# Optimization experiments

Measured on AMD Instinct MI355X. Metric: run time of the kernel, lower is better.

The kernel has to match this reference:

```python
import jax, jax.numpy as jnp
import numpy as np

B, L, E, H, D = 4, 2048, 2048, 16, 128
HALF = D // 2
EPS = 1e-6


def setup_inputs() -> dict:
    key = jax.random.key(0)
    ks = jax.random.split(key, 8)
    s = 1.0 / np.sqrt(E)
    x = jax.random.normal(ks[0], (B, L, E), dtype=jnp.float32)
    # causal boolean mask, True = attend
    attention_mask = jnp.tril(jnp.ones((L, L), dtype=bool))[None, None, :, :]
    attention_mask = jnp.broadcast_to(attention_mask, (B, 1, L, L))
    pos = jnp.arange(L, dtype=jnp.float32)[:, None]
    inv_freq = 1.0 / (10000.0 ** (jnp.arange(HALF, dtype=jnp.float32) / HALF))
    ang = pos * inv_freq[None, :]  # [L, HALF]
    cos = jnp.broadcast_to(jnp.cos(ang)[None], (B, L, HALF)).astype(jnp.float32)
    sin = jnp.broadcast_to(jnp.sin(ang)[None], (B, L, HALF)).astype(jnp.float32)
    Wq = jax.random.normal(ks[1], (H * D, E), dtype=jnp.float32) * s
    Wk = jax.random.normal(ks[2], (H * D, E), dtype=jnp.float32) * s
    Wv = jax.random.normal(ks[3], (H * D, E), dtype=jnp.float32) * s
    Wo = jax.random.normal(ks[4], (E, H * D), dtype=jnp.float32) * s
    q_norm_w = jnp.ones((D,), dtype=jnp.float32)
    k_norm_w = jnp.ones((D,), dtype=jnp.float32)
    return {"x": x, "attention_mask": attention_mask, "cos": cos, "sin": sin,
            "Wq": Wq, "Wk": Wk, "Wv": Wv, "Wo": Wo,
            "q_norm_w": q_norm_w, "k_norm_w": k_norm_w}


def _rmsnorm(t, w):
    # t: [B,H,L,D]; matches torch: x / sqrt(mean(x^2) + eps) * w
    ms = jnp.mean(t * t, axis=-1, keepdims=True)
    return w * (t * jax.lax.rsqrt(ms + EPS))


def _rope(t, cos, sin):
    # t: [B,H,L,D]; cos/sin: [B,L,HALF] -> [B,1,L,HALF]
    c = cos[:, None, :, :]
    s = sin[:, None, :, :]
    t1, t2 = t[..., :HALF], t[..., HALF:]
    return jnp.concatenate([t1 * c - t2 * s, t1 * s + t2 * c], axis=-1)


def reference(x, attention_mask, cos, sin, Wq, Wk, Wv, Wo, q_norm_w, k_norm_w):
    b, l, _ = x.shape
    q = (x @ Wq.T).reshape(b, l, H, D).transpose(0, 2, 1, 3)  # [B,H,L,D]
    k = (x @ Wk.T).reshape(b, l, H, D).transpose(0, 2, 1, 3)
    v = (x @ Wv.T).reshape(b, l, H, D).transpose(0, 2, 1, 3)
    q = _rope(_rmsnorm(q, q_norm_w), cos, sin)
    k = _rope(_rmsnorm(k, k_norm_w), cos, sin)
    scale = 1.0 / jnp.sqrt(jnp.asarray(D, dtype=x.dtype))
    scores = jnp.einsum('bhld,bhmd->bhlm', q, k) * scale  # [B,H,L,L]
    scores = jnp.where(attention_mask, scores, -jnp.inf)
    attn = jax.nn.softmax(scores, axis=-1)
    out = jnp.einsum('bhlm,bhmd->bhld', attn, v)  # [B,H,L,D]
    out = out.transpose(0, 2, 1, 3).reshape(b, l, H * D)
    return out @ Wo.T
```

## Files before the change

kernel.cpp:

```cpp
#include <hip/hip_runtime.h>
#include <hip/hip_bf16.h>
#include <stdint.h>

#define B_SZ 4
#define L_SEQ 2048
#define EMB 2048
#define NH 16
#define HD 128
#define BLROWS (B_SZ * L_SEQ)
#define BK 32

typedef __bf16 bf16;
typedef __bf16 bf16x8 __attribute__((ext_vector_type(8)));
typedef __bf16 bf16x4 __attribute__((ext_vector_type(4)));
typedef float f32x4 __attribute__((ext_vector_type(4)));

#define MFMA16(A, Bv, C) __builtin_amdgcn_mfma_f32_16x16x32_bf16(A, Bv, C, 0, 0, 0)

__device__ __forceinline__ void gll16(bf16* l, const bf16* g) {
  __builtin_amdgcn_global_load_lds(
      (const __attribute__((address_space(1))) unsigned int*)g,
      (__attribute__((address_space(3))) unsigned int*)l, 16, 0, 0);
}

__global__ __launch_bounds__(256) void f2b_kernel(const float* __restrict__ in,
                                                  bf16* __restrict__ out, int n4) {
  int i = blockIdx.x * blockDim.x + threadIdx.x;
  int stride = gridDim.x * blockDim.x;
  for (; i < n4; i += stride) {
    float4 v = ((const float4*)in)[i];
    bf16x4 o = {(bf16)v.x, (bf16)v.y, (bf16)v.z, (bf16)v.w};
    ((bf16x4*)out)[i] = o;
  }
}

__global__ __launch_bounds__(256) void f2bW_kernel(const float* __restrict__ w0,
                                                   const float* __restrict__ w1,
                                                   const float* __restrict__ w2,
                                                   const float* __restrict__ w3,
                                                   bf16* __restrict__ o0,
                                                   bf16* __restrict__ o1,
                                                   bf16* __restrict__ o2,
                                                   bf16* __restrict__ o3, int n4) {
  const float* in = (blockIdx.y == 0) ? w0 : (blockIdx.y == 1) ? w1
                    : (blockIdx.y == 2) ? w2 : w3;
  bf16* out = (blockIdx.y == 0) ? o0 : (blockIdx.y == 1) ? o1
              : (blockIdx.y == 2) ? o2 : o3;
  int i = blockIdx.x * blockDim.x + threadIdx.x;
  int stride = gridDim.x * blockDim.x;
  for (; i < n4; i += stride) {
    float4 v = ((const float4*)in)[i];
    bf16x4 o = {(bf16)v.x, (bf16)v.y, (bf16)v.z, (bf16)v.w};
    ((bf16x4*)out)[i] = o;
  }
}

template <int EPI, int BNT>
__global__ __launch_bounds__(512, 2) void gemm256(const bf16* __restrict__ A,
                                                  const bf16* __restrict__ Bm,
                                                  bf16* __restrict__ Cq,
                                                  bf16* __restrict__ Ck,
                                                  bf16* __restrict__ Cvt,
                                                  float* __restrict__ Cf,
                                                  int K) {
  constexpr int NB = BNT / 64;
  __shared__ bf16 Abuf[3][256 * BK];
  __shared__ bf16 Bbuf[3][BNT * BK];
  const int tid = threadIdx.x, lane = tid & 63, w = tid >> 6;
  const int wr = w >> 2, wc = w & 3;
  const int l15 = lane & 15;

  const int q8 = gridDim.x >> 3;
  const int wg = ((int)blockIdx.x & 7) * q8 + ((int)blockIdx.x >> 3);
  const int nbm = 32;
  const int bm = (wg & (nbm - 1)) * 256;
  const int bn = (wg / nbm) * BNT;
  const int NT = K / BK;

  const int idA0 = tid, idA1 = 512 + tid;
  const int ar0 = idA0 >> 2, ar1 = idA1 >> 2;
  const size_t aS0 = (size_t)(bm + ar0) * K + (((idA0 & 3) ^ ((ar0 >> 1) & 3)) * 8);
  const size_t aS1 = (size_t)(bm + ar1) * K + (((idA1 & 3) ^ ((ar1 >> 1) & 3)) * 8);
  const size_t bS0 = (size_t)(bn + ar0) * K + (((idA0 & 3) ^ ((ar0 >> 1) & 3)) * 8);
  const size_t bS1 = (size_t)(bn + ar1) * K + (((idA1 & 3) ^ ((ar1 >> 1) & 3)) * 8);
  const int ldsD0 = idA0 * 8, ldsD1 = idA1 * 8;

  const int eSw = ((lane >> 4) * 8) ^ (((l15 >> 1) & 3) << 3);
  int aoff[8], boff[NB];
#pragma unroll
  for (int m = 0; m < 8; m++) aoff[m] = (wr * 128 + m * 16 + l15) * BK + eSw;
#pragma unroll
  for (int n = 0; n < NB; n++) boff[n] = (wc * (BNT / 4) + n * 16 + l15) * BK + eSw;

  f32x4 acc[8][NB] = {};

  gll16(&Abuf[0][ldsD0], A + aS0);
  gll16(&Bbuf[0][ldsD0], Bm + bS0);
  gll16(&Abuf[0][ldsD1], A + aS1);
  if constexpr (BNT == 256) gll16(&Bbuf[0][ldsD1], Bm + bS1);
  gll16(&Abuf[1][ldsD0], A + aS0 + BK);
  gll16(&Bbuf[1][ldsD0], Bm + bS0 + BK);
  gll16(&Abuf[1][ldsD1], A + aS1 + BK);
  if constexpr (BNT == 256) gll16(&Bbuf[1][ldsD1], Bm + bS1 + BK);
  if constexpr (BNT == 256)
    asm volatile("s_waitcnt vmcnt(4)" ::: "memory");
  else
    asm volatile("s_waitcnt vmcnt(3)" ::: "memory");
  __builtin_amdgcn_s_barrier();
  asm volatile("" ::: "memory");

  int cur = 0, nxt = 2;
  for (int kt = 0; kt < NT; ++kt) {
    const bf16* __restrict__ Ab = Abuf[cur];
    const bf16* __restrict__ Bb = Bbuf[cur];
    const bool pre = (kt + 2 < NT);
    const size_t k2 = (size_t)(kt + 2) * BK;

    bf16x8 af[8], bq[NB];
#pragma unroll
    for (int m = 0; m < 8; m++) af[m] = *(const bf16x8*)&Ab[aoff[m]];
    bq[0] = *(const bf16x8*)&Bb[boff[0]];
    if constexpr (NB > 2) bq[1] = *(const bf16x8*)&Bb[boff[1]];
    if (pre) {
      gll16(&Abuf[nxt][ldsD0], A + aS0 + k2);
      gll16(&Bbuf[nxt][ldsD0], Bm + bS0 + k2);
    }
    asm volatile("s_waitcnt lgkmcnt(0)" ::: "memory");
    __builtin_amdgcn_sched_barrier(0);
    __builtin_amdgcn_s_setprio(1);
#pragma unroll
    for (int m = 0; m < 8; m++) acc[m][0] = MFMA16(af[m], bq[0], acc[m][0]);
    if constexpr (NB > 2) {
#pragma unroll
      for (int m = 0; m < 8; m++) acc[m][1] = MFMA16(af[m], bq[1], acc[m][1]);
    }
    __builtin_amdgcn_s_setprio(0);

    constexpr int n2 = (NB > 2) ? 2 : 1;
    bf16x8 b2 = *(const bf16x8*)&Bb[boff[n2]];
    bf16x8 b3;
    if constexpr (NB > 2) b3 = *(const bf16x8*)&Bb[boff[3]];
    if (pre) {
      gll16(&Abuf[nxt][ldsD1], A + aS1 + k2);
      if constexpr (BNT == 256) gll16(&Bbuf[nxt][ldsD1], Bm + bS1 + k2);
    }
    asm volatile("s_waitcnt lgkmcnt(0)" ::: "memory");
    __builtin_amdgcn_sched_barrier(0);
    __builtin_amdgcn_s_setprio(1);
#pragma unroll
    for (int m = 0; m < 8; m++) acc[m][n2] = MFMA16(af[m], b2, acc[m][n2]);
    if constexpr (NB > 2) {
#pragma unroll
      for (int m = 0; m < 8; m++) acc[m][3] = MFMA16(af[m], b3, acc[m][3]);
    }
    __builtin_amdgcn_s_setprio(0);

    if (kt < NT - 1) {
      if (pre) {
        if constexpr (BNT == 256)
          asm volatile("s_waitcnt vmcnt(4)" ::: "memory");
        else
          asm volatile("s_waitcnt vmcnt(3)" ::: "memory");
      } else {
        asm volatile("s_waitcnt vmcnt(0)" ::: "memory");
      }
      __builtin_amdgcn_s_barrier();
      asm volatile("" ::: "memory");
    }
    cur = (cur == 2) ? 0 : cur + 1;
    nxt = (nxt == 2) ? 0 : nxt + 1;
  }

  const int grow0 = bm + wr * 128 + (lane >> 4) * 4;
  const int gcol0 = bn + wc * (BNT / 4) + l15;
#pragma unroll
  for (int i = 0; i < 8; i++)
#pragma unroll
    for (int j = 0; j < NB; j++) {
      int grow = grow0 + i * 16;
      int gcol = gcol0 + j * 16;
      if (EPI == 1) {
#pragma unroll
        for (int r = 0; r < 4; r++)
          Cf[(size_t)(grow + r) * 2048 + gcol] = acc[i][j][r];
      } else {
        int mat = gcol >> 11, mcol = gcol & 2047;
        if (mat == 2) {
          int b = grow >> 11;
          bf16x4 pk = {(bf16)acc[i][j][0], (bf16)acc[i][j][1],
                       (bf16)acc[i][j][2], (bf16)acc[i][j][3]};
          *(bf16x4*)&Cvt[((size_t)(b * 2048 + mcol)) * 2048 + (grow & 2047)] = pk;
        } else {
          bf16* Cp = (mat == 0) ? Cq : Ck;
#pragma unroll
          for (int r = 0; r < 4; r++)
            Cp[(size_t)(grow + r) * 2048 + mcol] = (bf16)acc[i][j][r];
        }
      }
    }
}

__global__ __launch_bounds__(256) void normrope2_kernel(bf16* __restrict__ Tq,
                                                        bf16* __restrict__ Tk,
                                                        const float* __restrict__ wq,
                                                        const float* __restrict__ wk,
                                                        const float* __restrict__ cs,
                                                        const float* __restrict__ sn) {
  bf16* T = blockIdx.y ? Tk : Tq;
  const float* w = blockIdx.y ? wk : wq;
  int row = blockIdx.x * 4 + (threadIdx.x >> 6);
  int lane = threadIdx.x & 63;
  int bl = row >> 4;
  int h = row & 15;
  bf16* p = T + (size_t)bl * EMB + h * HD;
  float v1 = (float)p[lane];
  float v2 = (float)p[lane + 64];
  float ss = v1 * v1 + v2 * v2;
#pragma unroll
  for (int m = 32; m; m >>= 1) ss += __shfl_xor(ss, m, 64);
  float r = rsqrtf(ss * (1.0f / 128.0f) + 1e-6f);
  float n1 = v1 * r * w[lane];
  float n2 = v2 * r * w[lane + 64];
  float c = cs[(size_t)bl * 64 + lane];
  float s = sn[(size_t)bl * 64 + lane];
  p[lane]      = (bf16)(n1 * c - n2 * s);
  p[lane + 64] = (bf16)(n1 * s + n2 * c);
}

__device__ __forceinline__ void stage_kv(bf16* Ksb, bf16* Vsb,
                                         const bf16* gK, const bf16* gV,
                                         int kt, int w, int lane) {
#pragma unroll
  for (int i = 0; i < 4; i++) {
    int ck = i * 256 + w * 64 + lane;
    int kr = ck >> 4, kc = ck & 15;
    gll16(&Ksb[ck * 8], gK + (size_t)(kt * 64 + kr) * EMB + ((kc ^ (kr & 7)) * 8));
    int dr = ck >> 3, vc = ck & 7;
    gll16(&Vsb[ck * 8], gV + (size_t)dr * L_SEQ + kt * 64 + ((vc ^ (dr & 7)) * 8));
  }
}

__global__ __launch_bounds__(256) void fattn_kernel(const bf16* __restrict__ Q,
                                                    const bf16* __restrict__ K,
                                                    const bf16* __restrict__ Vt,
                                                    bf16* __restrict__ AO) {
  __shared__ bf16 Ks[2][64 * 128];
  __shared__ bf16 Vs[2][64 * 128];
  __shared__ bf16 Ps[4 * 16 * 64];
  const int tid = threadIdx.x, lane = tid & 63, w = tid >> 6;

  int id = blockIdx.x + blockIdx.y * 32;
  int bh = id & 63;
  int qt = 31 - (id >> 6);
  const int b = bh >> 4, h = bh & 15;
  const size_t base = (size_t)b * L_SEQ * EMB + h * HD;
  const bf16* gK = K + base;
  const bf16* gV = Vt + (size_t)(b * NH + h) * HD * L_SEQ;
  const int qrow0 = qt * 64 + w * 16;

  const float a_ = 0.08838834764831845f * 1.4426950408889634f;
  const float b_ = 12.0f * 1.4426950408889634f;

  bf16x8 qf[4];
  {
    const bf16* qp = Q + base + (size_t)(qrow0 + (lane & 15)) * EMB + ((lane >> 4) * 8);
#pragma unroll
    for (int c = 0; c < 4; c++) qf[c] = *(const bf16x8*)(qp + c * 32);
  }
  const bf16 one1 = (bf16)1.0f;
  const bf16x8 ones = {one1, one1, one1, one1, one1, one1, one1, one1};

  f32x4 O[8] = {};
  f32x4 lsum = {0.f, 0.f, 0.f, 0.f};
  const int qg0 = qrow0 + (lane >> 4) * 4;
  bf16* myP = Ps + w * 1024;

  stage_kv(Ks[0], Vs[0], gK, gV, 0, w, lane);
  asm volatile("s_waitcnt vmcnt(0)" ::: "memory");
  __builtin_amdgcn_s_barrier();
  asm volatile("" ::: "memory");

  for (int kt = 0; kt <= qt; kt++) {
    const int cur = kt & 1;
    if (kt < qt) stage_kv(Ks[cur ^ 1], Vs[cur ^ 1], gK, gV, kt + 1, w, lane);

    f32x4 S[4] = {};
    __builtin_amdgcn_s_setprio(1);
#pragma unroll
    for (int s = 0; s < 4; s++) {
      int row = s * 16 + (lane & 15);
#pragma unroll
      for (int c = 0; c < 4; c++) {
        int swc = (c * 4 + (lane >> 4)) ^ (row & 7);
        bf16x8 kf = *(const bf16x8*)&Ks[cur][row * 128 + swc * 8];
        S[s] = MFMA16(qf[c], kf, S[s]);
      }
    }
    __builtin_amdgcn_s_setprio(0);

    const bool diag = (kt == qt);
    const int prow = (lane >> 4) * 4;
#pragma unroll
    for (int s = 0; s < 4; s++) {
      int kg = kt * 64 + s * 16 + (lane & 15);
#pragma unroll
      for (int r = 0; r < 4; r++) {
        float e = exp2f(S[s][r] * a_ - b_);
        if (diag && kg > qg0 + r) e = 0.f;
        int row = prow + r;
        myP[(row * 64 + s * 16 + (lane & 15)) ^ ((row & 7) << 3)] = (bf16)e;
      }
    }
    bf16x8 pf[2];
#pragma unroll
    for (int kk = 0; kk < 2; kk++) {
      int row = lane & 15;
      int swc = (kk * 4 + (lane >> 4)) ^ (row & 7);
      pf[kk] = *(const bf16x8*)&myP[row * 64 + swc * 8];
    }
    __builtin_amdgcn_s_setprio(1);
    lsum = MFMA16(pf[0], ones, lsum);
    lsum = MFMA16(pf[1], ones, lsum);
#pragma unroll
    for (int ni = 0; ni < 8; ni++) {
#pragma unroll
      for (int kk = 0; kk < 2; kk++) {
        int drow = ni * 16 + (lane & 15);
        int swc = (kk * 4 + (lane >> 4)) ^ (drow & 7);
        bf16x8 vf = *(const bf16x8*)&Vs[cur][drow * 64 + swc * 8];
        O[ni] = MFMA16(pf[kk], vf, O[ni]);
      }
    }
    __builtin_amdgcn_s_setprio(0);

    asm volatile("s_waitcnt vmcnt(0)" ::: "memory");
    __builtin_amdgcn_s_barrier();
    asm volatile("" ::: "memory");
  }

#pragma unroll
  for (int ni = 0; ni < 8; ni++) {
#pragma unroll
    for (int r = 0; r < 4; r++) {
      float o = O[ni][r] / lsum[r];
      AO[(size_t)(b * L_SEQ + qg0 + r) * EMB + h * HD + ni * 16 + (lane & 15)] = (bf16)o;
    }
  }
}

extern "C" void kernel_launch(void* const* d_in, const int* in_sizes, int n_in,
                              void* d_out, int out_size, void* d_ws, size_t ws_size,
                              hipStream_t stream) {
  const float* x = (const float*)d_in[0];
  const float* cosp = (const float*)d_in[2];
  const float* sinp = (const float*)d_in[3];
  const float* Wq = (const float*)d_in[4];
  const float* Wk = (const float*)d_in[5];
  const float* Wv = (const float*)d_in[6];
  const float* Wo = (const float*)d_in[7];
  const float* qw = (const float*)d_in[8];
  const float* kw = (const float*)d_in[9];

  const size_t ACT = (size_t)BLROWS * EMB * sizeof(bf16);
  const size_t WGT = (size_t)EMB * EMB * sizeof(bf16);
  char* ws = (char*)d_ws;
  bf16* xb    = (bf16*)ws;          ws += ACT;
  bf16* WQKVb = (bf16*)ws;          ws += 3 * WGT;
  bf16* Wob   = (bf16*)ws;          ws += WGT;
  bf16* Qb    = (bf16*)ws;          ws += ACT;
  bf16* Kb    = (bf16*)ws;          ws += ACT;
  bf16* Vtb   = (bf16*)ws;          ws += ACT;
  bf16* AOb   = (bf16*)ws;          ws += ACT;

  f2b_kernel<<<2048, 256, 0, stream>>>(x, xb, BLROWS * EMB / 4);
  f2bW_kernel<<<dim3(512, 4), 256, 0, stream>>>(
      Wq, Wk, Wv, Wo, WQKVb, WQKVb + (size_t)EMB * EMB,
      WQKVb + 2 * (size_t)EMB * EMB, Wob, EMB * EMB / 4);

  gemm256<0, 256><<<768, 512, 0, stream>>>(xb, WQKVb, Qb, Kb, Vtb, nullptr, EMB);

  normrope2_kernel<<<dim3(BLROWS * NH / 4, 2), 256, 0, stream>>>(Qb, Kb, qw, kw,
                                                                 cosp, sinp);

  fattn_kernel<<<dim3(32, B_SZ * NH), 256, 0, stream>>>(Qb, Kb, Vtb, AOb);

  gemm256<1, 128><<<512, 512, 0, stream>>>(AOb, Wob, nullptr, nullptr, nullptr,
                                           (float*)d_out, EMB);
}
```

Baseline: 478.8 us.

## Keep attention P in registers, deepen QKV GEMM pipeline, merge conversion kernels

The attention kernel now computes S transposed (K as the A operand), so each lane holds its P values in registers and feeds them straight into a 16x16x16 bf16 MFMA against V. This drops the per-warp LDS round trip for P and the ones-MFMA row-sum, which is replaced by a per-lane running sum reduced with shuffles at the end. The QKV GEMM gets a 4-stage LDS pipeline with a prefetch distance of 3, and the fp32-to-bf16 conversions for x and the weights are merged into one launch. In exchange, LDS use in the GEMM grows and the attention kernel issues twice as many smaller-K MFMAs for PV.

```diff
diff --git a/kernel.cpp b/kernel.cpp
--- a/kernel.cpp
+++ b/kernel.cpp
@@ -14,8 +14,23 @@
 typedef __bf16 bf16x8 __attribute__((ext_vector_type(8)));
 typedef __bf16 bf16x4 __attribute__((ext_vector_type(4)));
 typedef float f32x4 __attribute__((ext_vector_type(4)));
+typedef short short4v __attribute__((ext_vector_type(4)));
 
 #define MFMA16(A, Bv, C) __builtin_amdgcn_mfma_f32_16x16x32_bf16(A, Bv, C, 0, 0, 0)
+
+__device__ __forceinline__ f32x4 mfma16k16(bf16x4 a, bf16x4 b, f32x4 c) {
+#if __has_builtin(__builtin_amdgcn_mfma_f32_16x16x16bf16_1k)
+  return __builtin_amdgcn_mfma_f32_16x16x16bf16_1k(
+      __builtin_bit_cast(short4v, a), __builtin_bit_cast(short4v, b), c, 0, 0, 0);
+#else
+  f32x4 d = c;
+  asm volatile("v_mfma_f32_16x16x16_bf16 %0, %1, %2, %0"
+               : "+v"(d)
+               : "v"(__builtin_bit_cast(short4v, a)),
+                 "v"(__builtin_bit_cast(short4v, b)));
+  return d;
+#endif
+}
 
 __device__ __forceinline__ void gll16(bf16* l, const bf16* g) {
   __builtin_amdgcn_global_load_lds(
@@ -23,8 +38,18 @@
       (__attribute__((address_space(3))) unsigned int*)l, 16, 0, 0);
 }
 
-__global__ __launch_bounds__(256) void f2b_kernel(const float* __restrict__ in,
-                                                  bf16* __restrict__ out, int n4) {
+__global__ __launch_bounds__(256) void f2bAll_kernel(
+    const float* __restrict__ x, const float* __restrict__ w0,
+    const float* __restrict__ w1, const float* __restrict__ w2,
+    const float* __restrict__ w3, bf16* __restrict__ ox, bf16* __restrict__ o0,
+    bf16* __restrict__ o1, bf16* __restrict__ o2, bf16* __restrict__ o3,
+    int nx4, int nw4) {
+  const int y = blockIdx.y;
+  const float* in = (y == 0) ? x : (y == 1) ? w0 : (y == 2) ? w1
+                    : (y == 3) ? w2 : w3;
+  bf16* out = (y == 0) ? ox : (y == 1) ? o0 : (y == 2) ? o1
+              : (y == 3) ? o2 : o3;
+  const int n4 = (y == 0) ? nx4 : nw4;
   int i = blockIdx.x * blockDim.x + threadIdx.x;
   int stride = gridDim.x * blockDim.x;
   for (; i < n4; i += stride) {
@@ -34,28 +59,7 @@
   }
 }
 
-__global__ __launch_bounds__(256) void f2bW_kernel(const float* __restrict__ w0,
-                                                   const float* __restrict__ w1,
-                                                   const float* __restrict__ w2,
-                                                   const float* __restrict__ w3,
-                                                   bf16* __restrict__ o0,
-                                                   bf16* __restrict__ o1,
-                                                   bf16* __restrict__ o2,
-                                                   bf16* __restrict__ o3, int n4) {
-  const float* in = (blockIdx.y == 0) ? w0 : (blockIdx.y == 1) ? w1
-                    : (blockIdx.y == 2) ? w2 : w3;
-  bf16* out = (blockIdx.y == 0) ? o0 : (blockIdx.y == 1) ? o1
-              : (blockIdx.y == 2) ? o2 : o3;
-  int i = blockIdx.x * blockDim.x + threadIdx.x;
-  int stride = gridDim.x * blockDim.x;
-  for (; i < n4; i += stride) {
-    float4 v = ((const float4*)in)[i];
-    bf16x4 o = {(bf16)v.x, (bf16)v.y, (bf16)v.z, (bf16)v.w};
-    ((bf16x4*)out)[i] = o;
-  }
-}
-
-template <int EPI, int BNT>
+template <int EPI, int BNT, int ST>
 __global__ __launch_bounds__(512, 2) void gemm256(const bf16* __restrict__ A,
                                                   const bf16* __restrict__ Bm,
                                                   bf16* __restrict__ Cq,
@@ -64,8 +68,8 @@
                                                   float* __restrict__ Cf,
                                                   int K) {
   constexpr int NB = BNT / 64;
-  __shared__ bf16 Abuf[3][256 * BK];
-  __shared__ bf16 Bbuf[3][BNT * BK];
+  __shared__ bf16 Abuf[ST][256 * BK];
+  __shared__ bf16 Bbuf[ST][BNT * BK];
   const int tid = threadIdx.x, lane = tid & 63, w = tid >> 6;
   const int wr = w >> 2, wc = w & 3;
   const int l15 = lane & 15;
@@ -94,27 +98,40 @@
 
   f32x4 acc[8][NB] = {};
 
-  gll16(&Abuf[0][ldsD0], A + aS0);
-  gll16(&Bbuf[0][ldsD0], Bm + bS0);
-  gll16(&Abuf[0][ldsD1], A + aS1);
-  if constexpr (BNT == 256) gll16(&Bbuf[0][ldsD1], Bm + bS1);
-  gll16(&Abuf[1][ldsD0], A + aS0 + BK);
-  gll16(&Bbuf[1][ldsD0], Bm + bS0 + BK);
-  gll16(&Abuf[1][ldsD1], A + aS1 + BK);
-  if constexpr (BNT == 256) gll16(&Bbuf[1][ldsD1], Bm + bS1 + BK);
-  if constexpr (BNT == 256)
-    asm volatile("s_waitcnt vmcnt(4)" ::: "memory");
-  else
-    asm volatile("s_waitcnt vmcnt(3)" ::: "memory");
+  if constexpr (ST == 4) {
+#pragma unroll
+    for (int t0 = 0; t0 < 3; t0++) {
+      gll16(&Abuf[t0][ldsD0], A + aS0 + t0 * BK);
+      gll16(&Bbuf[t0][ldsD0], Bm + bS0 + t0 * BK);
+      gll16(&Abuf[t0][ldsD1], A + aS1 + t0 * BK);
+      gll16(&Bbuf[t0][ldsD1], Bm + bS1 + t0 * BK);
+    }
+    asm volatile("s_waitcnt vmcnt(8)" ::: "memory");
+  } else {
+    gll16(&Abuf[0][ldsD0], A + aS0);
+    gll16(&Bbuf[0][ldsD0], Bm + bS0);
+    gll16(&Abuf[0][ldsD1], A + aS1);
+    if constexpr (BNT == 256) gll16(&Bbuf[0][ldsD1], Bm + bS1);
+    gll16(&Abuf[1][ldsD0], A + aS0 + BK);
+    gll16(&Bbuf[1][ldsD0], Bm + bS0 + BK);
+    gll16(&Abuf[1][ldsD1], A + aS1 + BK);
+    if constexpr (BNT == 256) gll16(&Bbuf[1][ldsD1], Bm + bS1 + BK);
+    if constexpr (BNT == 256)
+      asm volatile("s_waitcnt vmcnt(4)" ::: "memory");
+    else
+      asm volatile("s_waitcnt vmcnt(3)" ::: "memory");
+  }
   __builtin_amdgcn_s_barrier();
   asm volatile("" ::: "memory");
 
-  int cur = 0, nxt = 2;
   for (int kt = 0; kt < NT; ++kt) {
+    const int cur = (ST == 4) ? (kt & 3) : (kt % 3);
+    const int nxt = (ST == 4) ? ((kt + 3) & 3) : ((kt + 2) % 3);
     const bf16* __restrict__ Ab = Abuf[cur];
     const bf16* __restrict__ Bb = Bbuf[cur];
-    const bool pre = (kt + 2 < NT);
-    const size_t k2 = (size_t)(kt + 2) * BK;
+    const int pd = (ST == 4) ? 3 : 2;
+    const bool pre = (kt + pd < NT);
+    const size_t kp = (size_t)(kt + pd) * BK;
 
     bf16x8 af[8], bq[NB];
 #pragma unroll
@@ -122,8 +139,8 @@
     bq[0] = *(const bf16x8*)&Bb[boff[0]];
     if constexpr (NB > 2) bq[1] = *(const bf16x8*)&Bb[boff[1]];
     if (pre) {
-      gll16(&Abuf[nxt][ldsD0], A + aS0 + k2);
-      gll16(&Bbuf[nxt][ldsD0], Bm + bS0 + k2);
+      gll16(&Abuf[nxt][ldsD0], A + aS0 + kp);
+      gll16(&Bbuf[nxt][ldsD0], Bm + bS0 + kp);
     }
     asm volatile("s_waitcnt lgkmcnt(0)" ::: "memory");
     __builtin_amdgcn_sched_barrier(0);
@@ -141,8 +158,8 @@
     bf16x8 b3;
     if constexpr (NB > 2) b3 = *(const bf16x8*)&Bb[boff[3]];
     if (pre) {
-      gll16(&Abuf[nxt][ldsD1], A + aS1 + k2);
-      if constexpr (BNT == 256) gll16(&Bbuf[nxt][ldsD1], Bm + bS1 + k2);
+      gll16(&Abuf[nxt][ldsD1], A + aS1 + kp);
+      if constexpr (BNT == 256) gll16(&Bbuf[nxt][ldsD1], Bm + bS1 + kp);
     }
     asm volatile("s_waitcnt lgkmcnt(0)" ::: "memory");
     __builtin_amdgcn_sched_barrier(0);
@@ -156,19 +173,26 @@
     __builtin_amdgcn_s_setprio(0);
 
     if (kt < NT - 1) {
-      if (pre) {
-        if constexpr (BNT == 256)
+      if constexpr (ST == 4) {
+        if (kt + 3 < NT)
+          asm volatile("s_waitcnt vmcnt(8)" ::: "memory");
+        else if (kt + 2 < NT)
           asm volatile("s_waitcnt vmcnt(4)" ::: "memory");
         else
-          asm volatile("s_waitcnt vmcnt(3)" ::: "memory");
+          asm volatile("s_waitcnt vmcnt(0)" ::: "memory");
       } else {
-        asm volatile("s_waitcnt vmcnt(0)" ::: "memory");
+        if (pre) {
+          if constexpr (BNT == 256)
+            asm volatile("s_waitcnt vmcnt(4)" ::: "memory");
+          else
+            asm volatile("s_waitcnt vmcnt(3)" ::: "memory");
+        } else {
+          asm volatile("s_waitcnt vmcnt(0)" ::: "memory");
+        }
       }
       __builtin_amdgcn_s_barrier();
       asm volatile("" ::: "memory");
     }
-    cur = (cur == 2) ? 0 : cur + 1;
-    nxt = (nxt == 2) ? 0 : nxt + 1;
   }
 
   const int grow0 = bm + wr * 128 + (lane >> 4) * 4;
@@ -246,8 +270,8 @@
                                                     bf16* __restrict__ AO) {
   __shared__ bf16 Ks[2][64 * 128];
   __shared__ bf16 Vs[2][64 * 128];
-  __shared__ bf16 Ps[4 * 16 * 64];
   const int tid = threadIdx.x, lane = tid & 63, w = tid >> 6;
+  const int l15 = lane & 15, grp = lane >> 4;
 
   int id = blockIdx.x + blockIdx.y * 32;
   int bh = id & 63;
@@ -257,23 +281,20 @@
   const bf16* gK = K + base;
   const bf16* gV = Vt + (size_t)(b * NH + h) * HD * L_SEQ;
   const int qrow0 = qt * 64 + w * 16;
+  const int q_own = qrow0 + l15;
 
   const float a_ = 0.08838834764831845f * 1.4426950408889634f;
   const float b_ = 12.0f * 1.4426950408889634f;
 
   bf16x8 qf[4];
   {
-    const bf16* qp = Q + base + (size_t)(qrow0 + (lane & 15)) * EMB + ((lane >> 4) * 8);
+    const bf16* qp = Q + base + (size_t)(qrow0 + l15) * EMB + (grp * 8);
 #pragma unroll
     for (int c = 0; c < 4; c++) qf[c] = *(const bf16x8*)(qp + c * 32);
   }
-  const bf16 one1 = (bf16)1.0f;
-  const bf16x8 ones = {one1, one1, one1, one1, one1, one1, one1, one1};
 
   f32x4 O[8] = {};
-  f32x4 lsum = {0.f, 0.f, 0.f, 0.f};
-  const int qg0 = qrow0 + (lane >> 4) * 4;
-  bf16* myP = Ps + w * 1024;
+  float lsum_p = 0.f;
 
   stage_kv(Ks[0], Vs[0], gK, gV, 0, w, lane);
   asm volatile("s_waitcnt vmcnt(0)" ::: "memory");
@@ -284,51 +305,46 @@
     const int cur = kt & 1;
     if (kt < qt) stage_kv(Ks[cur ^ 1], Vs[cur ^ 1], gK, gV, kt + 1, w, lane);
 
-    f32x4 S[4] = {};
+    f32x4 st[4] = {};
     __builtin_amdgcn_s_setprio(1);
 #pragma unroll
     for (int s = 0; s < 4; s++) {
-      int row = s * 16 + (lane & 15);
+      int row = s * 16 + l15;
 #pragma unroll
       for (int c = 0; c < 4; c++) {
-        int swc = (c * 4 + (lane >> 4)) ^ (row & 7);
+        int swc = (c * 4 + grp) ^ (row & 7);
         bf16x8 kf = *(const bf16x8*)&Ks[cur][row * 128 + swc * 8];
-        S[s] = MFMA16(qf[c], kf, S[s]);
+        st[s] = MFMA16(kf, qf[c], st[s]);
       }
     }
     __builtin_amdgcn_s_setprio(0);
 
     const bool diag = (kt == qt);
-    const int prow = (lane >> 4) * 4;
+    bf16x4 pk[4];
 #pragma unroll
     for (int s = 0; s < 4; s++) {
-      int kg = kt * 64 + s * 16 + (lane & 15);
+      float e[4];
 #pragma unroll
       for (int r = 0; r < 4; r++) {
-        float e = exp2f(S[s][r] * a_ - b_);
-        if (diag && kg > qg0 + r) e = 0.f;
-        int row = prow + r;
-        myP[(row * 64 + s * 16 + (lane & 15)) ^ ((row & 7) << 3)] = (bf16)e;
+        int kg = kt * 64 + s * 16 + grp * 4 + r;
+        float v = exp2f(st[s][r] * a_ - b_);
+        if (diag && kg > q_own) v = 0.f;
+        e[r] = v;
+        lsum_p += v;
       }
-    }
-    bf16x8 pf[2];
-#pragma unroll
-    for (int kk = 0; kk < 2; kk++) {
-      int row = lane & 15;
-      int swc = (kk * 4 + (lane >> 4)) ^ (row & 7);
-      pf[kk] = *(const bf16x8*)&myP[row * 64 + swc * 8];
-    }
+      pk[s] = bf16x4{(bf16)e[0], (bf16)e[1], (bf16)e[2], (bf16)e[3]};
+    }
+
     __builtin_amdgcn_s_setprio(1);
-    lsum = MFMA16(pf[0], ones, lsum);
-    lsum = MFMA16(pf[1], ones, lsum);
 #pragma unroll
     for (int ni = 0; ni < 8; ni++) {
-#pragma unroll
-      for (int kk = 0; kk < 2; kk++) {
-        int drow = ni * 16 + (lane & 15);
-        int swc = (kk * 4 + (lane >> 4)) ^ (drow & 7);
-        bf16x8 vf = *(const bf16x8*)&Vs[cur][drow * 64 + swc * 8];
-        O[ni] = MFMA16(pf[kk], vf, O[ni]);
+      int drow = ni * 16 + l15;
+#pragma unroll
+      for (int s = 0; s < 4; s++) {
+        int chunk = s * 2 + (grp >> 1);
+        int eoff = ((chunk ^ (drow & 7)) << 3) + (grp & 1) * 4;
+        bf16x4 vf = *(const bf16x4*)&Vs[cur][drow * 64 + eoff];
+        O[ni] = mfma16k16(pk[s], vf, O[ni]);
       }
     }
     __builtin_amdgcn_s_setprio(0);
@@ -338,12 +354,19 @@
     asm volatile("" ::: "memory");
   }
 
+  lsum_p += __shfl_xor(lsum_p, 16, 64);
+  lsum_p += __shfl_xor(lsum_p, 32, 64);
+  float lr[4];
+#pragma unroll
+  for (int r = 0; r < 4; r++) lr[r] = __shfl(lsum_p, grp * 4 + r, 64);
+
 #pragma unroll
   for (int ni = 0; ni < 8; ni++) {
 #pragma unroll
     for (int r = 0; r < 4; r++) {
-      float o = O[ni][r] / lsum[r];
-      AO[(size_t)(b * L_SEQ + qg0 + r) * EMB + h * HD + ni * 16 + (lane & 15)] = (bf16)o;
+      float o = O[ni][r] / lr[r];
+      int grow = qrow0 + grp * 4 + r;
+      AO[(size_t)(b * L_SEQ + grow) * EMB + h * HD + ni * 16 + l15] = (bf16)o;
     }
   }
 }
@@ -372,18 +395,17 @@
   bf16* Vtb   = (bf16*)ws;          ws += ACT;
   bf16* AOb   = (bf16*)ws;          ws += ACT;
 
-  f2b_kernel<<<2048, 256, 0, stream>>>(x, xb, BLROWS * EMB / 4);
-  f2bW_kernel<<<dim3(512, 4), 256, 0, stream>>>(
-      Wq, Wk, Wv, Wo, WQKVb, WQKVb + (size_t)EMB * EMB,
-      WQKVb + 2 * (size_t)EMB * EMB, Wob, EMB * EMB / 4);
-
-  gemm256<0, 256><<<768, 512, 0, stream>>>(xb, WQKVb, Qb, Kb, Vtb, nullptr, EMB);
+  f2bAll_kernel<<<dim3(512, 5), 256, 0, stream>>>(
+      x, Wq, Wk, Wv, Wo, xb, WQKVb, WQKVb + (size_t)EMB * EMB,
+      WQKVb + 2 * (size_t)EMB * EMB, Wob, BLROWS * EMB / 4, EMB * EMB / 4);
+
+  gemm256<0, 256, 4><<<768, 512, 0, stream>>>(xb, WQKVb, Qb, Kb, Vtb, nullptr, EMB);
 
   normrope2_kernel<<<dim3(BLROWS * NH / 4, 2), 256, 0, stream>>>(Qb, Kb, qw, kw,
                                                                  cosp, sinp);
 
   fattn_kernel<<<dim3(32, B_SZ * NH), 256, 0, stream>>>(Qb, Kb, Vtb, AOb);
 
-  gemm256<1, 128><<<512, 512, 0, stream>>>(AOb, Wob, nullptr, nullptr, nullptr,
-                                           (float*)d_out, EMB);
-}
+  gemm256<1, 128, 3><<<512, 512, 0, stream>>>(AOb, Wob, nullptr, nullptr, nullptr,
+                                              (float*)d_out, EMB);
+}
```

Result: slower. 495.6 us (+3.5%).
